# Performance work log

Measured on AMD Instinct MI355X. Metric: run time of the kernel, lower is better.

## Reference

```python
import jax, jax.numpy as jnp
import numpy as np
from jax import lax

TOP_K = 2

def setup_inputs() -> dict:
    key = jax.random.key(0)
    ks = jax.random.split(key, 4)
    B, S = 4, 4096
    E, I1, I2, O1, O2 = 256, 32, 32, 32, 32
    x = jax.random.normal(ks[0], (B, S, I1 * I2), dtype=jnp.float32)
    router_w = jax.random.normal(ks[1], (E, I1 * I2), dtype=jnp.float32) / np.sqrt(I1 * I2)
    A_experts = jax.random.normal(ks[2], (E, O1, I1), dtype=jnp.float32)
    B_experts = jax.random.normal(ks[3], (E, O2, I2), dtype=jnp.float32)
    scale = jnp.ones((1,), dtype=jnp.float32)
    bias = jnp.zeros((O1 * O2,), dtype=jnp.float32)
    return {"x": x, "router_w": router_w, "A_experts": A_experts,
            "B_experts": B_experts, "scale": scale, "bias": bias}

def reference(x, router_w, A_experts, B_experts, scale, bias):
    E, O1, I1 = A_experts.shape
    _, O2, I2 = B_experts.shape
    x_flat = x.reshape(-1, I1 * I2)                      # [N, i1*i2]
    logits = x_flat @ router_w.T                         # [N, E]
    top_vals, top_idx = lax.top_k(logits, TOP_K)         # [N, k]
    top_probs = jax.nn.softmax(top_vals, axis=-1)        # [N, k]
    x_sub = x_flat.reshape(-1, I1, I2)                   # [N, i1, i2]
    A_g = A_experts[top_idx]                             # [N, k, o1, i1]
    B_g = B_experts[top_idx]                             # [N, k, o2, i2]
    # Kronecker bilinear: Y[n,k] = A_g[n,k] @ x_sub[n] @ B_g[n,k]^T
    Y = jnp.einsum('nkoi,nij,nkpj->nkop', A_g, x_sub, B_g)
    out = jnp.einsum('nkop,nk->nop', Y, top_probs)       # weighted combine
    out = out.reshape(*x.shape[:-1], O1 * O2)
    return out * scale + bias
```

## Files before the change

kernel.cpp:

```cpp
#include <hip/hip_runtime.h>
#include <math.h>

#define KD 1024
#define ED 256

typedef __attribute__((ext_vector_type(8)))  short s16x8;
typedef __attribute__((ext_vector_type(4)))  float f32x4;
typedef __attribute__((ext_vector_type(16))) float f32x16;

__device__ __forceinline__ short f2bf(float f) {
    union { float f; unsigned u; } v; v.f = f;
    unsigned r = v.u + 0x7fffu + ((v.u >> 16) & 1u);
    return (short)(r >> 16);
}
__device__ __forceinline__ float bf2f(short s) {
    union { unsigned u; float f; } v; v.u = ((unsigned)(unsigned short)s) << 16;
    return v.f;
}

__global__ __launch_bounds__(256)
void wconv_kernel(const float* __restrict__ w, short* __restrict__ wb, int n4) {
    int i = blockIdx.x * 256 + threadIdx.x;
    if (i < n4) {
        float4 v = ((const float4*)w)[i];
        short4 o;
        o.x = f2bf(v.x); o.y = f2bf(v.y); o.z = f2bf(v.z); o.w = f2bf(v.w);
        ((short4*)wb)[i] = o;
    }
}

__global__ __launch_bounds__(256)
void router_mfma(const float* __restrict__ x, const short* __restrict__ wb,
                 int* __restrict__ cand)
{
    __shared__ __align__(16) char smem[36864];
    char* XsB = smem;
    char* WsB = smem + 4096;
    float* Ls = (float*)smem;

    const int tid  = threadIdx.x;
    const int lane = tid & 63;
    const int wv   = tid >> 6;
    const int n0   = blockIdx.x * 32;

    f32x4 acc[2][4];
    #pragma unroll
    for (int i = 0; i < 2; ++i)
        #pragma unroll
        for (int j = 0; j < 4; ++j)
            #pragma unroll
            for (int r = 0; r < 4; ++r) acc[i][j][r] = 0.f;

    const int stok = tid >> 3;
    const int skq  = (tid & 7) * 8;
    const int xswz = (stok & 7) << 4;

    for (int ch = 0; ch < 16; ++ch) {
        {
            const float* xp = x + (size_t)(n0 + stok) * KD + ch * 64 + skq;
            float4 a = *(const float4*)xp;
            float4 b = *(const float4*)(xp + 4);
            s16x8 pk;
            pk[0] = f2bf(a.x); pk[1] = f2bf(a.y); pk[2] = f2bf(a.z); pk[3] = f2bf(a.w);
            pk[4] = f2bf(b.x); pk[5] = f2bf(b.y); pk[6] = f2bf(b.z); pk[7] = f2bf(b.w);
            *(s16x8*)(XsB + stok * 128 + ((skq * 2) ^ xswz)) = pk;
        }
        #pragma unroll
        for (int p = 0; p < 8; ++p) {
            const int e = p * 32 + stok % 32;
            s16x8 v = *(const s16x8*)(wb + (size_t)e * KD + ch * 64 + skq);
            *(s16x8*)(WsB + e * 128 + ((skq * 2) ^ ((e & 7) << 4))) = v;
        }
        __syncthreads();
        #pragma unroll
        for (int ks = 0; ks < 2; ++ks) {
            const int kbyte = ks * 64 + (lane >> 4) * 16;
            s16x8 af[2];
            #pragma unroll
            for (int fm = 0; fm < 2; ++fm) {
                const int tok = fm * 16 + (lane & 15);
                af[fm] = *(const s16x8*)(XsB + tok * 128 + (kbyte ^ ((tok & 7) << 4)));
            }
            #pragma unroll
            for (int fn = 0; fn < 4; ++fn) {
                const int e = wv * 64 + fn * 16 + (lane & 15);
                s16x8 bf = *(const s16x8*)(WsB + e * 128 + (kbyte ^ ((e & 7) << 4)));
                #pragma unroll
                for (int fm = 0; fm < 2; ++fm)
                    acc[fm][fn] = __builtin_amdgcn_mfma_f32_16x16x32_bf16(
                        af[fm], bf, acc[fm][fn], 0, 0, 0);
            }
        }
        __syncthreads();
    }

    #pragma unroll
    for (int fm = 0; fm < 2; ++fm)
        #pragma unroll
        for (int fn = 0; fn < 4; ++fn)
            #pragma unroll
            for (int r = 0; r < 4; ++r) {
                const int tok = fm * 16 + (lane >> 4) * 4 + r;
                const int e   = wv * 64 + fn * 16 + (lane & 15);
                Ls[tok * 260 + e] = acc[fm][fn][r];
            }
    __syncthreads();

    const int t = tid >> 3;
    const int s = tid & 7;
    float vv[8]; int ee[8];
    #pragma unroll
    for (int i = 0; i < 8; ++i) { vv[i] = -INFINITY; ee[i] = 0x7fffffff; }
    for (int q = 0; q < 32; ++q) {
        float tv = Ls[t * 260 + s * 32 + q];
        int   te = s * 32 + q;
        if ((tv > vv[7]) || (tv == vv[7] && te < ee[7])) {
            #pragma unroll
            for (int i = 0; i < 8; ++i) {
                bool g = (tv > vv[i]) || (tv == vv[i] && te < ee[i]);
                float fv = g ? vv[i] : tv; int fe = g ? ee[i] : te;
                vv[i] = g ? tv : vv[i];    ee[i] = g ? te : ee[i];
                tv = fv; te = fe;
            }
        }
    }
    int cnt = 0;
    #pragma unroll
    for (int it = 0; it < 8; ++it) {
        float cv = vv[0]; int ce = ee[0];
        #pragma unroll
        for (int i = 1; i < 8; ++i) {
            bool b = (cnt == i); cv = b ? vv[i] : cv; ce = b ? ee[i] : ce;
        }
        float bv = cv; int be = ce;
        #pragma unroll
        for (int m = 1; m <= 4; m <<= 1) {
            float ov = __shfl_xor(bv, m, 64);
            int   oe = __shfl_xor(be, m, 64);
            bool g = (ov > bv) || (ov == bv && oe < be);
            bv = g ? ov : bv; be = g ? oe : be;
        }
        if ((be >> 5) == s) cnt++;
        if (s == 0) cand[(size_t)(n0 + t) * 8 + it] = be;
    }
}

__global__ __launch_bounds__(512)
void refine8_kernel(const float* __restrict__ x, const float* __restrict__ w,
                    const int* __restrict__ cand, int* __restrict__ ridx,
                    float* __restrict__ rprob)
{
    const int tid  = threadIdx.x;
    const int wv   = tid >> 6;
    const int lane = tid & 63;
    const int n    = blockIdx.x * 8 + wv;

    int ce[8];
    #pragma unroll
    for (int c = 0; c < 8; ++c) ce[c] = cand[(size_t)n * 8 + c];

    const float* xr = x + (size_t)n * KD;
    float xf[16];
    #pragma unroll
    for (int i = 0; i < 16; ++i) xf[i] = xr[lane + i * 64];

    double acc[8];
    #pragma unroll
    for (int c = 0; c < 8; ++c) {
        const float* wr = w + (size_t)ce[c] * KD;
        double a = 0.0;
        #pragma unroll
        for (int i = 0; i < 16; ++i)
            a += (double)xf[i] * (double)wr[lane + i * 64];
        acc[c] = a;
    }
    #pragma unroll
    for (int c = 0; c < 8; ++c) {
        #pragma unroll
        for (int m = 32; m >= 1; m >>= 1) acc[c] += __shfl_xor(acc[c], m, 64);
    }
    if (lane == 0) {
        double b0 = -1e300, b1 = -1e300; int i0 = 0x7fffffff, i1 = 0x7fffffff;
        #pragma unroll
        for (int i = 0; i < 8; ++i) {
            double v = acc[i]; int ei = ce[i];
            if (v > b0 || (v == b0 && ei < i0)) { b1 = b0; i1 = i0; b0 = v; i0 = ei; }
            else if (v > b1 || (v == b1 && ei < i1)) { b1 = v; i1 = ei; }
        }
        double ex = exp(b1 - b0);
        ridx[n * 2 + 0] = i0; ridx[n * 2 + 1] = i1;
        rprob[n * 2 + 0] = (float)(1.0 / (1.0 + ex));
        rprob[n * 2 + 1] = (float)(ex / (1.0 + ex));
    }
}

__global__ __launch_bounds__(256)
void expert_mfma(const float* __restrict__ x, const float* __restrict__ Ae,
                 const float* __restrict__ Be, const int* __restrict__ ridx,
                 const float* __restrict__ rprob, const float* __restrict__ scale,
                 const float* __restrict__ bias, float* __restrict__ out)
{
    __shared__ __align__(16) float Ts[4][32 * 36];
    __shared__ __align__(16) float Sb[4][32 * 36];
    const int tid = threadIdx.x, lane = tid & 63, wv = tid >> 6;
    const int n = blockIdx.x * 4 + wv;
    const int col = lane & 31, hi = lane >> 5;
    float* sb = Sb[wv];
    float* ts = Ts[wv];

    const float* xr = x + (size_t)n * KD;
    #pragma unroll
    for (int it = 0; it < 4; ++it) {
        const int idx = it * 64 + lane;
        float4 v = *(const float4*)(xr + idx * 4);
        *(float4*)&sb[(idx >> 3) * 36 + (idx & 7) * 4] = v;
    }
    asm volatile("s_waitcnt lgkmcnt(0)" ::: "memory");
    s16x8 Xh[2], Xl[2];
    #pragma unroll
    for (int ks = 0; ks < 2; ++ks)
        #pragma unroll
        for (int j = 0; j < 8; ++j) {
            float v = sb[(ks * 16 + hi * 8 + j) * 36 + col];
            short h = f2bf(v);
            Xh[ks][j] = h;
            Xl[ks][j] = f2bf(v - bf2f(h));
        }

    f32x16 accY;
    #pragma unroll
    for (int r = 0; r < 16; ++r) accY[r] = 0.f;

    #pragma unroll
    for (int t = 0; t < 2; ++t) {
        const int   ei = ridx[(size_t)n * 2 + t];
        const float p  = rprob[(size_t)n * 2 + t];
        const float* ap = Ae + (size_t)ei * 1024;
        const float* bp = Be + (size_t)ei * 1024;

        #pragma unroll
        for (int it = 0; it < 4; ++it) {
            const int idx = it * 64 + lane;
            float4 v = *(const float4*)(ap + idx * 4);
            *(float4*)&sb[(idx >> 3) * 36 + (idx & 7) * 4] = v;
        }
        asm volatile("s_waitcnt lgkmcnt(0)" ::: "memory");
        s16x8 Ah[2], Al[2];
        #pragma unroll
        for (int ks = 0; ks < 2; ++ks) {
            float4 a0 = *(const float4*)&sb[col * 36 + ks * 16 + hi * 8];
            float4 a1 = *(const float4*)&sb[col * 36 + ks * 16 + hi * 8 + 4];
            const float av[8] = {a0.x, a0.y, a0.z, a0.w, a1.x, a1.y, a1.z, a1.w};
            #pragma unroll
            for (int j = 0; j < 8; ++j) {
                short h = f2bf(av[j]);
                Ah[ks][j] = h; Al[ks][j] = f2bf(av[j] - bf2f(h));
            }
        }
        #pragma unroll
        for (int it = 0; it < 4; ++it) {
            const int idx = it * 64 + lane;
            float4 v = *(const float4*)(bp + idx * 4);
            *(float4*)&sb[(idx >> 3) * 36 + (idx & 7) * 4] = v;
        }
        asm volatile("s_waitcnt lgkmcnt(0)" ::: "memory");
        s16x8 Bh[2], Bl[2];
        #pragma unroll
        for (int ks = 0; ks < 2; ++ks) {
            float4 b0 = *(const float4*)&sb[col * 36 + ks * 16 + hi * 8];
            float4 b1 = *(const float4*)&sb[col * 36 + ks * 16 + hi * 8 + 4];
            const float bw[8] = {b0.x, b0.y, b0.z, b0.w, b1.x, b1.y, b1.z, b1.w};
            #pragma unroll
            for (int j = 0; j < 8; ++j) {
                short h = f2bf(bw[j]);
                Bh[ks][j] = h; Bl[ks][j] = f2bf(bw[j] - bf2f(h));
            }
        }
        f32x16 accT;
        #pragma unroll
        for (int r = 0; r < 16; ++r) accT[r] = 0.f;
        #pragma unroll
        for (int ks = 0; ks < 2; ++ks) {
            accT = __builtin_amdgcn_mfma_f32_32x32x16_bf16(Ah[ks], Xh[ks], accT, 0, 0, 0);
            accT = __builtin_amdgcn_mfma_f32_32x32x16_bf16(Ah[ks], Xl[ks], accT, 0, 0, 0);
            accT = __builtin_amdgcn_mfma_f32_32x32x16_bf16(Al[ks], Xh[ks], accT, 0, 0, 0);
        }
        #pragma unroll
        for (int r = 0; r < 16; ++r) {
            const int o = (r & 3) + 8 * (r >> 2) + 4 * hi;
            ts[o * 36 + col] = accT[r] * p;
        }
        asm volatile("s_waitcnt lgkmcnt(0)" ::: "memory");
        s16x8 Th[2], Tl[2];
        #pragma unroll
        for (int ks = 0; ks < 2; ++ks) {
            float4 t0 = *(const float4*)&ts[col * 36 + ks * 16 + hi * 8];
            float4 t1 = *(const float4*)&ts[col * 36 + ks * 16 + hi * 8 + 4];
            const float tw[8] = {t0.x, t0.y, t0.z, t0.w, t1.x, t1.y, t1.z, t1.w};
            #pragma unroll
            for (int j = 0; j < 8; ++j) {
                short h = f2bf(tw[j]);
                Th[ks][j] = h; Tl[ks][j] = f2bf(tw[j] - bf2f(h));
            }
        }
        #pragma unroll
        for (int ks = 0; ks < 2; ++ks) {
            accY = __builtin_amdgcn_mfma_f32_32x32x16_bf16(Th[ks], Bh[ks], accY, 0, 0, 0);
            accY = __builtin_amdgcn_mfma_f32_32x32x16_bf16(Tl[ks], Bh[ks], accY, 0, 0, 0);
            accY = __builtin_amdgcn_mfma_f32_32x32x16_bf16(Th[ks], Bl[ks], accY, 0, 0, 0);
        }
    }
    const float scl = scale[0];
    float* orow = out + (size_t)n * KD;
    #pragma unroll
    for (int r = 0; r < 16; ++r) {
        const int o = (r & 3) + 8 * (r >> 2) + 4 * hi;
        orow[o * 32 + col] = accY[r] * scl + bias[o * 32 + col];
    }
}

extern "C" void kernel_launch(void* const* d_in, const int* in_sizes, int n_in,
                              void* d_out, int out_size, void* d_ws, size_t ws_size,
                              hipStream_t stream)
{
    const float* x     = (const float*)d_in[0];
    const float* rw    = (const float*)d_in[1];
    const float* Ae    = (const float*)d_in[2];
    const float* Be    = (const float*)d_in[3];
    const float* scale = (const float*)d_in[4];
    const float* bias  = (const float*)d_in[5];
    float* out = (float*)d_out;

    const int N = in_sizes[0] / KD;

    short* wbf  = (short*)d_ws;
    int*   cand = (int*)((char*)d_ws + (size_t)ED * KD * 2);
    int*   ridx = cand + (size_t)N * 8;
    float* rprob = (float*)(ridx + (size_t)N * 2);

    wconv_kernel<<<(ED * KD / 4 + 255) / 256, 256, 0, stream>>>(rw, wbf, ED * KD / 4);
    router_mfma<<<N / 32, 256, 0, stream>>>(x, wbf, cand);
    refine8_kernel<<<N / 8, 512, 0, stream>>>(x, rw, cand, ridx, rprob);
    expert_mfma<<<N / 4, 256, 0, stream>>>(x, Ae, Be, ridx, rprob, scale, bias, out);
}
```

Baseline: 237.8 us.

## Split router experts across two blocks, double-buffer LDS, and merge top-4 per half

The router GEMM now launches two blocks per 32-token tile, each covering 128 experts, so there are twice as many blocks. LDS is double-buffered so the next chunk's global loads overlap the current MFMAs, which removes one barrier per iteration. Top-8 selection becomes top-4 per half, merged with a shuffle-based merge network. The change of candidate semantics (top-4 from each half instead of a global top-8) still contains the global top-2, but it re-reads x twice and alters the candidate set passed to refine.

```diff
diff --git a/kernel.cpp b/kernel.cpp
--- a/kernel.cpp
+++ b/kernel.cpp
@@ -33,115 +33,152 @@
 void router_mfma(const float* __restrict__ x, const short* __restrict__ wb,
                  int* __restrict__ cand)
 {
-    __shared__ __align__(16) char smem[36864];
-    char* XsB = smem;
-    char* WsB = smem + 4096;
+    __shared__ __align__(16) char smem[40960];
+    char* Wbase = smem;
+    char* Xbase = smem + 32768;
     float* Ls = (float*)smem;
 
     const int tid  = threadIdx.x;
     const int lane = tid & 63;
     const int wv   = tid >> 6;
-    const int n0   = blockIdx.x * 32;
-
-    f32x4 acc[2][4];
+    const int bid  = blockIdx.x;
+    const int n0   = (bid >> 1) * 32;
+    const int half = bid & 1;
+    const int e0   = half * 128;
+
+    f32x4 acc[2][2];
     #pragma unroll
     for (int i = 0; i < 2; ++i)
         #pragma unroll
-        for (int j = 0; j < 4; ++j)
+        for (int j = 0; j < 2; ++j)
             #pragma unroll
             for (int r = 0; r < 4; ++r) acc[i][j][r] = 0.f;
 
-    const int stok = tid >> 3;
-    const int skq  = (tid & 7) * 8;
-    const int xswz = (stok & 7) << 4;
-
+    const int wrow = tid >> 3;
+    const int b16  = (tid & 7) * 16;
+    const int k8   = (tid & 7) * 8;
+    const int wswz = (wrow & 7) << 4;
+
+    {
+        s16x8 wreg[4];
+        #pragma unroll
+        for (int q = 0; q < 4; ++q)
+            wreg[q] = *(const s16x8*)(wb + (size_t)(e0 + wrow + q * 32) * KD + (tid & 7) * 8);
+        const float* xp = x + (size_t)(n0 + wrow) * KD + k8;
+        float4 xa = *(const float4*)xp;
+        float4 xb = *(const float4*)(xp + 4);
+        #pragma unroll
+        for (int q = 0; q < 4; ++q)
+            *(s16x8*)(Wbase + (wrow + q * 32) * 128 + (b16 ^ wswz)) = wreg[q];
+        s16x8 pk;
+        pk[0]=f2bf(xa.x); pk[1]=f2bf(xa.y); pk[2]=f2bf(xa.z); pk[3]=f2bf(xa.w);
+        pk[4]=f2bf(xb.x); pk[5]=f2bf(xb.y); pk[6]=f2bf(xb.z); pk[7]=f2bf(xb.w);
+        *(s16x8*)(Xbase + wrow * 128 + ((k8 * 2) ^ wswz)) = pk;
+    }
+    __syncthreads();
+
+    int cur = 0;
+    const int frow = lane & 15;
+    const int fswz = (lane & 7) << 4;
     for (int ch = 0; ch < 16; ++ch) {
-        {
-            const float* xp = x + (size_t)(n0 + stok) * KD + ch * 64 + skq;
-            float4 a = *(const float4*)xp;
-            float4 b = *(const float4*)(xp + 4);
+        char* Wc = Wbase + cur * 16384;
+        char* Xc = Xbase + cur * 4096;
+        char* Wn = Wbase + (cur ^ 1) * 16384;
+        char* Xn = Xbase + (cur ^ 1) * 4096;
+        const bool pf = (ch < 15);
+
+        s16x8 wreg[4];
+        float4 xa, xb;
+        if (pf) {
+            const int ch1 = ch + 1;
+            #pragma unroll
+            for (int q = 0; q < 4; ++q)
+                wreg[q] = *(const s16x8*)(wb + (size_t)(e0 + wrow + q * 32) * KD + ch1 * 64 + (tid & 7) * 8);
+            const float* xp = x + (size_t)(n0 + wrow) * KD + ch1 * 64 + k8;
+            xa = *(const float4*)xp;
+            xb = *(const float4*)(xp + 4);
+        }
+
+        #pragma unroll
+        for (int ks = 0; ks < 2; ++ks) {
+            const int kb  = ks * 64 + (lane >> 4) * 16;
+            const int kbs = kb ^ fswz;
+            s16x8 af0 = *(const s16x8*)(Xc + frow * 128 + kbs);
+            s16x8 af1 = *(const s16x8*)(Xc + (16 + frow) * 128 + kbs);
+            s16x8 bf0 = *(const s16x8*)(Wc + (wv * 32 + frow) * 128 + kbs);
+            s16x8 bf1 = *(const s16x8*)(Wc + (wv * 32 + 16 + frow) * 128 + kbs);
+            acc[0][0] = __builtin_amdgcn_mfma_f32_16x16x32_bf16(af0, bf0, acc[0][0], 0, 0, 0);
+            acc[0][1] = __builtin_amdgcn_mfma_f32_16x16x32_bf16(af0, bf1, acc[0][1], 0, 0, 0);
+            acc[1][0] = __builtin_amdgcn_mfma_f32_16x16x32_bf16(af1, bf0, acc[1][0], 0, 0, 0);
+            acc[1][1] = __builtin_amdgcn_mfma_f32_16x16x32_bf16(af1, bf1, acc[1][1], 0, 0, 0);
+        }
+
+        if (pf) {
+            #pragma unroll
+            for (int q = 0; q < 4; ++q)
+                *(s16x8*)(Wn + (wrow + q * 32) * 128 + (b16 ^ wswz)) = wreg[q];
             s16x8 pk;
-            pk[0] = f2bf(a.x); pk[1] = f2bf(a.y); pk[2] = f2bf(a.z); pk[3] = f2bf(a.w);
-            pk[4] = f2bf(b.x); pk[5] = f2bf(b.y); pk[6] = f2bf(b.z); pk[7] = f2bf(b.w);
-            *(s16x8*)(XsB + stok * 128 + ((skq * 2) ^ xswz)) = pk;
-        }
-        #pragma unroll
-        for (int p = 0; p < 8; ++p) {
-            const int e = p * 32 + stok % 32;
-            s16x8 v = *(const s16x8*)(wb + (size_t)e * KD + ch * 64 + skq);
-            *(s16x8*)(WsB + e * 128 + ((skq * 2) ^ ((e & 7) << 4))) = v;
+            pk[0]=f2bf(xa.x); pk[1]=f2bf(xa.y); pk[2]=f2bf(xa.z); pk[3]=f2bf(xa.w);
+            pk[4]=f2bf(xb.x); pk[5]=f2bf(xb.y); pk[6]=f2bf(xb.z); pk[7]=f2bf(xb.w);
+            *(s16x8*)(Xn + wrow * 128 + ((k8 * 2) ^ wswz)) = pk;
         }
         __syncthreads();
-        #pragma unroll
-        for (int ks = 0; ks < 2; ++ks) {
-            const int kbyte = ks * 64 + (lane >> 4) * 16;
-            s16x8 af[2];
-            #pragma unroll
-            for (int fm = 0; fm < 2; ++fm) {
-                const int tok = fm * 16 + (lane & 15);
-                af[fm] = *(const s16x8*)(XsB + tok * 128 + (kbyte ^ ((tok & 7) << 4)));
-            }
-            #pragma unroll
-            for (int fn = 0; fn < 4; ++fn) {
-                const int e = wv * 64 + fn * 16 + (lane & 15);
-                s16x8 bf = *(const s16x8*)(WsB + e * 128 + (kbyte ^ ((e & 7) << 4)));
-                #pragma unroll
-                for (int fm = 0; fm < 2; ++fm)
-                    acc[fm][fn] = __builtin_amdgcn_mfma_f32_16x16x32_bf16(
-                        af[fm], bf, acc[fm][fn], 0, 0, 0);
-            }
-        }
-        __syncthreads();
+        cur ^= 1;
     }
 
     #pragma unroll
     for (int fm = 0; fm < 2; ++fm)
         #pragma unroll
-        for (int fn = 0; fn < 4; ++fn)
+        for (int fn = 0; fn < 2; ++fn)
             #pragma unroll
             for (int r = 0; r < 4; ++r) {
                 const int tok = fm * 16 + (lane >> 4) * 4 + r;
-                const int e   = wv * 64 + fn * 16 + (lane & 15);
-                Ls[tok * 260 + e] = acc[fm][fn][r];
+                const int e   = wv * 32 + fn * 16 + (lane & 15);
+                Ls[tok * 132 + e] = acc[fm][fn][r];
             }
     __syncthreads();
 
-    const int t = tid >> 3;
-    const int s = tid & 7;
-    float vv[8]; int ee[8];
-    #pragma unroll
-    for (int i = 0; i < 8; ++i) { vv[i] = -INFINITY; ee[i] = 0x7fffffff; }
-    for (int q = 0; q < 32; ++q) {
-        float tv = Ls[t * 260 + s * 32 + q];
-        int   te = s * 32 + q;
-        if ((tv > vv[7]) || (tv == vv[7] && te < ee[7])) {
-            #pragma unroll
-            for (int i = 0; i < 8; ++i) {
-                bool g = (tv > vv[i]) || (tv == vv[i] && te < ee[i]);
-                float fv = g ? vv[i] : tv; int fe = g ? ee[i] : te;
-                vv[i] = g ? tv : vv[i];    ee[i] = g ? te : ee[i];
-                tv = fv; te = fe;
-            }
-        }
-    }
-    int cnt = 0;
-    #pragma unroll
-    for (int it = 0; it < 8; ++it) {
-        float cv = vv[0]; int ce = ee[0];
-        #pragma unroll
-        for (int i = 1; i < 8; ++i) {
-            bool b = (cnt == i); cv = b ? vv[i] : cv; ce = b ? ee[i] : ce;
-        }
-        float bv = cv; int be = ce;
-        #pragma unroll
-        for (int m = 1; m <= 4; m <<= 1) {
-            float ov = __shfl_xor(bv, m, 64);
-            int   oe = __shfl_xor(be, m, 64);
-            bool g = (ov > bv) || (ov == bv && oe < be);
-            bv = g ? ov : bv; be = g ? oe : be;
-        }
-        if ((be >> 5) == s) cnt++;
-        if (s == 0) cand[(size_t)(n0 + t) * 8 + it] = be;
+    const int t8 = tid >> 3;
+    const int sg = tid & 7;
+    float vv0=-INFINITY, vv1=-INFINITY, vv2=-INFINITY, vv3=-INFINITY;
+    int   ee0=0x7fffffff, ee1=0x7fffffff, ee2=0x7fffffff, ee3=0x7fffffff;
+    #pragma unroll
+    for (int q = 0; q < 16; ++q) {
+        const float tv = Ls[t8 * 132 + sg * 16 + q];
+        const int   te = sg * 16 + q;
+        if ((tv > vv3) || (tv == vv3 && te < ee3)) {
+            const bool g0 = (tv > vv0) || (tv == vv0 && te < ee0);
+            const bool g1 = (tv > vv1) || (tv == vv1 && te < ee1);
+            const bool g2 = (tv > vv2) || (tv == vv2 && te < ee2);
+            if (g0)      { vv3=vv2;ee3=ee2; vv2=vv1;ee2=ee1; vv1=vv0;ee1=ee0; vv0=tv;ee0=te; }
+            else if (g1) { vv3=vv2;ee3=ee2; vv2=vv1;ee2=ee1; vv1=tv;ee1=te; }
+            else if (g2) { vv3=vv2;ee3=ee2; vv2=tv;ee2=te; }
+            else         { vv3=tv;ee3=te; }
+        }
+    }
+    #pragma unroll
+    for (int m = 1; m <= 4; m <<= 1) {
+        const float u0=__shfl_xor(vv0,m,64), u1=__shfl_xor(vv1,m,64),
+                    u2=__shfl_xor(vv2,m,64), u3=__shfl_xor(vv3,m,64);
+        const int   f0=__shfl_xor(ee0,m,64), f1=__shfl_xor(ee1,m,64),
+                    f2=__shfl_xor(ee2,m,64), f3=__shfl_xor(ee3,m,64);
+        float av[4]={vv0,vv1,vv2,vv3}, bv[4]={u0,u1,u2,u3};
+        int   ae[4]={ee0,ee1,ee2,ee3}, be[4]={f0,f1,f2,f3};
+        float rv[4]; int re[4]; int pa=0, pb=0;
+        #pragma unroll
+        for (int k2 = 0; k2 < 4; ++k2) {
+            const float va=av[pa], vb=bv[pb];
+            const int   ia=ae[pa], ib=be[pb];
+            const bool ta = (va > vb) || (va == vb && ia < ib);
+            rv[k2] = ta ? va : vb; re[k2] = ta ? ia : ib;
+            pa += ta ? 1 : 0; pb += ta ? 0 : 1;
+        }
+        vv0=rv[0];vv1=rv[1];vv2=rv[2];vv3=rv[3];
+        ee0=re[0];ee1=re[1];ee2=re[2];ee3=re[3];
+    }
+    if (sg == 0) {
+        int* cp = cand + (size_t)(n0 + t8) * 8 + half * 4;
+        cp[0] = e0 + ee0; cp[1] = e0 + ee1; cp[2] = e0 + ee2; cp[3] = e0 + ee3;
     }
 }
 
@@ -339,7 +376,7 @@
     float* rprob = (float*)(ridx + (size_t)N * 2);
 
     wconv_kernel<<<(ED * KD / 4 + 255) / 256, 256, 0, stream>>>(rw, wbf, ED * KD / 4);
-    router_mfma<<<N / 32, 256, 0, stream>>>(x, wbf, cand);
+    router_mfma<<<(N / 32) * 2, 256, 0, stream>>>(x, wbf, cand);
     refine8_kernel<<<N / 8, 512, 0, stream>>>(x, rw, cand, ridx, rprob);
     expert_mfma<<<N / 4, 256, 0, stream>>>(x, Ae, Be, ridx, rprob, scale, bias, out);
 }
```

Result: faster. 206.6 us (-13.1%).
